# Kernel optimization log

Hardware: AMD Instinct MI355X
Metric: run time of the kernel (lower is better)

## Reference

```python
import jax, jax.numpy as jnp
import numpy as np
import math

B, T, D = 2, 2048, 1024
H, HS = 16, 64  # n_heads, head_size; D == H*HS


def setup_inputs() -> dict:
    key = jax.random.key(0)
    k1, k2, k3 = jax.random.split(key, 3)
    x = jax.random.normal(k1, (B, T, D), dtype=jnp.float32)
    w_qkv = jax.random.normal(k2, (D, 3 * D), dtype=jnp.float32) * (1.0 / math.sqrt(D))
    b_qkv = jnp.zeros((3 * D,), dtype=jnp.float32)
    w_out = jax.random.normal(k3, (D, D), dtype=jnp.float32) * (1.0 / math.sqrt(D))
    b_out = jnp.zeros((D,), dtype=jnp.float32)
    return {"x": x, "w_qkv": w_qkv, "b_qkv": b_qkv, "w_out": w_out, "b_out": b_out}


def reference(x, w_qkv, b_qkv, w_out, b_out):
    b, t, d = x.shape
    qkv = x @ w_qkv + b_qkv                       # (B,T,3D)
    q, k, v = jnp.split(qkv, 3, axis=-1)
    # (B,T,D) -> (B,H,T,HS)
    q = q.reshape(b, t, H, HS).transpose(0, 2, 1, 3)
    k = k.reshape(b, t, H, HS).transpose(0, 2, 1, 3)
    v = v.reshape(b, t, H, HS).transpose(0, 2, 1, 3)
    scale = 1.0 / math.sqrt(HS)
    attn = jnp.einsum('bhqd,bhkd->bhqk', q, k) * scale  # (B,H,T,T)
    causal = jnp.tril(jnp.ones((t, t), dtype=bool))
    attn = jnp.where(causal[None, None], attn, -jnp.inf)
    attn = jax.nn.softmax(attn, axis=-1)
    o = jnp.einsum('bhqk,bhkd->bhqd', attn, v)          # (B,H,T,HS)
    o = o.transpose(0, 2, 1, 3).reshape(b, t, d)
    return o @ w_out + b_out
```

## Files before the change

### kernel.cpp

```cpp
#include <hip/hip_runtime.h>
#include <math.h>

#define B_  2
#define T_  2048
#define D_  1024
#define H_  16
#define HS_ 64
#define M_  (B_*T_)

typedef __bf16 bf16x8 __attribute__((ext_vector_type(8)));
typedef float  f32x4  __attribute__((ext_vector_type(4)));
typedef unsigned short u16;

static __device__ __forceinline__ u16 f2bf(float f) {
    unsigned int u = __float_as_uint(f);
    u += 0x7fff + ((u >> 16) & 1);
    return (u16)(u >> 16);
}

static __device__ __forceinline__ void glds16(const u16* g, u16* l) {
    __builtin_amdgcn_global_load_lds(
        (const __attribute__((address_space(1))) void*)g,
        (__attribute__((address_space(3))) void*)l, 16, 0, 0);
}

static __device__ __forceinline__ bf16x8 lds_chunk(const u16* base, int row, int c) {
    return *reinterpret_cast<const bf16x8*>(base + (size_t)(row * 8 + (c ^ (row & 7))) * 8);
}

__global__ void cast_kernel(const float* __restrict__ in, u16* __restrict__ out) {
    int i = (blockIdx.x * blockDim.x + threadIdx.x) * 4;
    float4 v = *reinterpret_cast<const float4*>(in + i);
    ushort4 o;
    o.x = f2bf(v.x); o.y = f2bf(v.y); o.z = f2bf(v.z); o.w = f2bf(v.w);
    *reinterpret_cast<ushort4*>(out + i) = o;
}

__global__ void transpose_cast(const float* __restrict__ in, u16* __restrict__ out,
                               int R, int C) {
    __shared__ float tile[32][33];
    int c0 = blockIdx.x * 32, r0 = blockIdx.y * 32;
    int tx = threadIdx.x, ty = threadIdx.y;
    #pragma unroll
    for (int j = 0; j < 4; ++j)
        tile[ty + j*8][tx] = in[(size_t)(r0 + ty + j*8) * C + c0 + tx];
    __syncthreads();
    #pragma unroll
    for (int j = 0; j < 4; ++j)
        out[(size_t)(c0 + ty + j*8) * R + r0 + tx] = f2bf(tile[tx][ty + j*8]);
}

template<int MODE>
__global__ __launch_bounds__(256) void gemm_bt(
    const u16* __restrict__ A, const u16* __restrict__ Bt,
    const float* __restrict__ bias,
    float* __restrict__ Cf,
    u16* __restrict__ Qb, u16* __restrict__ Kb, u16* __restrict__ Vt,
    int M, int N, int K)
{
    __shared__ u16 As[128 * 64];
    __shared__ u16 Bs[128 * 64];
    int tid  = threadIdx.x;
    int lane = tid & 63, wave = tid >> 6;
    int wm = wave >> 1, wn = wave & 1;
    int quad = lane >> 4, lr = lane & 15;
    int bm = blockIdx.x, bn = blockIdx.y;

    f32x4 acc[4][4] = {};

    const u16* Ab = A  + (size_t)(bm * 128) * K;
    const u16* Bb = Bt + (size_t)(bn * 128) * K;

    int srow = tid >> 3;
    int scol = ((tid & 7) ^ (srow & 7)) * 8;

    for (int k0 = 0; k0 < K; k0 += 64) {
        __syncthreads();
        #pragma unroll
        for (int t = 0; t < 4; ++t)
            glds16(Ab + (size_t)(srow + 32*t) * K + k0 + scol, As + (size_t)(tid + 256*t) * 8);
        #pragma unroll
        for (int t = 0; t < 4; ++t)
            glds16(Bb + (size_t)(srow + 32*t) * K + k0 + scol, Bs + (size_t)(tid + 256*t) * 8);
        __syncthreads();
        #pragma unroll
        for (int kk = 0; kk < 2; ++kk) {
            bf16x8 af[4], bfr[4];
            int c = kk * 4 + quad;
            #pragma unroll
            for (int i = 0; i < 4; ++i)
                af[i] = lds_chunk(As, wm*64 + i*16 + lr, c);
            #pragma unroll
            for (int j = 0; j < 4; ++j)
                bfr[j] = lds_chunk(Bs, wn*64 + j*16 + lr, c);
            #pragma unroll
            for (int i = 0; i < 4; ++i)
                #pragma unroll
                for (int j = 0; j < 4; ++j)
                    acc[i][j] = __builtin_amdgcn_mfma_f32_16x16x32_bf16(af[i], bfr[j], acc[i][j], 0, 0, 0);
        }
    }

    #pragma unroll
    for (int i = 0; i < 4; ++i) {
        int mrow = bm*128 + wm*64 + i*16 + quad*4;
        #pragma unroll
        for (int j = 0; j < 4; ++j) {
            int ncol = bn*128 + wn*64 + j*16 + lr;
            float bv = bias[ncol];
            #pragma unroll
            for (int r = 0; r < 4; ++r) {
                float v = acc[i][j][r] + bv;
                int m = mrow + r;
                if (MODE == 1) {
                    Cf[(size_t)m * N + ncol] = v;
                } else {
                    int b = m >> 11, t = m & (T_ - 1);
                    int s = ncol >> 10, rem = ncol & 1023;
                    int h = rem >> 6, d = rem & 63;
                    int bh = b * H_ + h;
                    if (s == 0)      Qb[((size_t)bh*T_ + t)*HS_ + d] = f2bf(v * 0.125f);
                    else if (s == 1) Kb[((size_t)bh*T_ + t)*HS_ + d] = f2bf(v);
                    else             Vt[((size_t)bh*HS_ + d)*T_ + t] = f2bf(v);
                }
            }
        }
    }
}

__global__ __launch_bounds__(256) void attn_kernel(
    const u16* __restrict__ Qb, const u16* __restrict__ Kb,
    const u16* __restrict__ Vt, u16* __restrict__ Ob)
{
    __shared__ u16 Ks[64 * 64];
    __shared__ u16 Vs[64 * 64];
    __shared__ u16 Ps[4][32 * 64];

    int tid  = threadIdx.x;
    int lane = tid & 63, wave = tid >> 6;
    int quad = lane >> 4, lr = lane & 15;

    int lin = blockIdx.x;
    int bh  = (lin & 7) + 8 * ((lin >> 3) & 3);
    int p   = lin >> 5;

    int grp  = wave >> 1;
    int wg   = wave & 1;
    int myst = grp ? (31 - p) : p;
    int qb   = myst * 64 + wg * 32;
    int jd   = myst;
    int jmax = 31 - p;

    bf16x8 qf[2][2];
    #pragma unroll
    for (int mi = 0; mi < 2; ++mi)
        #pragma unroll
        for (int h2 = 0; h2 < 2; ++h2)
            qf[mi][h2] = *reinterpret_cast<const bf16x8*>(
                Qb + ((size_t)bh*T_ + qb + mi*16 + lr)*HS_ + h2*32 + quad*8);

    f32x4 Oa[2][4] = {};
    float lrow[2][4] = {};

    int srow = tid >> 3;
    int scol = ((tid & 7) ^ (srow & 7)) * 8;
    const u16* Kst0 = Kb + ((size_t)bh*T_ + srow     )*HS_ + scol;
    const u16* Kst1 = Kb + ((size_t)bh*T_ + srow + 32)*HS_ + scol;
    const u16* Vst0 = Vt + ((size_t)bh*HS_ + srow     )*T_ + scol;
    const u16* Vst1 = Vt + ((size_t)bh*HS_ + srow + 32)*T_ + scol;

    bf16x8 kpre0 = *reinterpret_cast<const bf16x8*>(Kst0);
    bf16x8 kpre1 = *reinterpret_cast<const bf16x8*>(Kst1);
    bf16x8 vpre0 = *reinterpret_cast<const bf16x8*>(Vst0);
    bf16x8 vpre1 = *reinterpret_cast<const bf16x8*>(Vst1);

    for (int jt = 0; jt <= jmax; ++jt) {
        __syncthreads();
        reinterpret_cast<bf16x8*>(Ks)[tid]       = kpre0;
        reinterpret_cast<bf16x8*>(Ks)[tid + 256] = kpre1;
        reinterpret_cast<bf16x8*>(Vs)[tid]       = vpre0;
        reinterpret_cast<bf16x8*>(Vs)[tid + 256] = vpre1;
        if (jt < jmax) {
            size_t kn = (size_t)(jt + 1) * 64;
            kpre0 = *reinterpret_cast<const bf16x8*>(Kst0 + kn * HS_);
            kpre1 = *reinterpret_cast<const bf16x8*>(Kst1 + kn * HS_);
            vpre0 = *reinterpret_cast<const bf16x8*>(Vst0 + kn);
            vpre1 = *reinterpret_cast<const bf16x8*>(Vst1 + kn);
        }
        __syncthreads();

        if (jt <= jd) {
            int kb = jt * 64;
            f32x4 Sa[2][4] = {};
            #pragma unroll
            for (int kk = 0; kk < 2; ++kk) {
                int c = kk * 4 + quad;
                #pragma unroll
                for (int nt = 0; nt < 4; ++nt) {
                    bf16x8 bk = lds_chunk(Ks, nt*16 + lr, c);
                    #pragma unroll
                    for (int mi = 0; mi < 2; ++mi)
                        Sa[mi][nt] = __builtin_amdgcn_mfma_f32_16x16x32_bf16(
                            qf[mi][kk], bk, Sa[mi][nt], 0, 0, 0);
                }
            }

            if (jt == jd) {
                #pragma unroll
                for (int mi = 0; mi < 2; ++mi)
                    #pragma unroll
                    for (int nt = 0; nt < 4; ++nt)
                        #pragma unroll
                        for (int r = 0; r < 4; ++r) {
                            int kg = kb + nt*16 + lr;
                            int qg = qb + mi*16 + quad*4 + r;
                            if (kg > qg) Sa[mi][nt][r] = -INFINITY;
                        }
            }

            #pragma unroll
            for (int mi = 0; mi < 2; ++mi)
                #pragma unroll
                for (int nt = 0; nt < 4; ++nt)
                    #pragma unroll
                    for (int r = 0; r < 4; ++r) {
                        float pv = __expf(Sa[mi][nt][r]);
                        lrow[mi][r] += pv;
                        int prow = mi*16 + quad*4 + r;
                        int c = nt*2 + (lr >> 3);
                        Ps[wave][(size_t)(prow*8 + (c ^ (prow & 7)))*8 + (lr & 7)] = f2bf(pv);
                    }

            #pragma unroll
            for (int kk = 0; kk < 2; ++kk) {
                int c = kk * 4 + quad;
                bf16x8 pa[2];
                #pragma unroll
                for (int mi = 0; mi < 2; ++mi)
                    pa[mi] = lds_chunk(Ps[wave], mi*16 + lr, c);
                #pragma unroll
                for (int nt = 0; nt < 4; ++nt) {
                    bf16x8 vb = lds_chunk(Vs, nt*16 + lr, c);
                    #pragma unroll
                    for (int mi = 0; mi < 2; ++mi)
                        Oa[mi][nt] = __builtin_amdgcn_mfma_f32_16x16x32_bf16(
                            pa[mi], vb, Oa[mi][nt], 0, 0, 0);
                }
            }
        }
    }

    int b = bh >> 4, h = bh & 15;
    #pragma unroll
    for (int mi = 0; mi < 2; ++mi)
        #pragma unroll
        for (int r = 0; r < 4; ++r) {
            float s = lrow[mi][r];
            #pragma unroll
            for (int off = 8; off >= 1; off >>= 1)
                s += __shfl_xor(s, off, 64);
            float inv = 1.f / s;
            int qg = qb + mi*16 + quad*4 + r;
            #pragma unroll
            for (int nt = 0; nt < 4; ++nt) {
                int d = nt*16 + lr;
                Ob[((size_t)b*T_ + qg)*D_ + h*HS_ + d] = f2bf(Oa[mi][nt][r] * inv);
            }
        }
}

extern "C" void kernel_launch(void* const* d_in, const int* in_sizes, int n_in,
                              void* d_out, int out_size, void* d_ws, size_t ws_size,
                              hipStream_t stream) {
    (void)in_sizes; (void)n_in; (void)out_size; (void)ws_size;
    const float* x     = (const float*)d_in[0];
    const float* w_qkv = (const float*)d_in[1];
    const float* b_qkv = (const float*)d_in[2];
    const float* w_out = (const float*)d_in[3];
    const float* b_out = (const float*)d_in[4];
    float* out = (float*)d_out;

    char* ws = (char*)d_ws;
    u16* Xb    = (u16*)ws; ws += (size_t)M_ * D_ * 2;
    u16* WqkvT = (u16*)ws; ws += (size_t)3 * D_ * D_ * 2;
    u16* WoutT = (u16*)ws; ws += (size_t)D_ * D_ * 2;
    u16* Qb    = (u16*)ws; ws += (size_t)M_ * D_ * 2;
    u16* Kb    = (u16*)ws; ws += (size_t)M_ * D_ * 2;
    u16* Vt    = (u16*)ws; ws += (size_t)M_ * D_ * 2;
    u16* Ob    = (u16*)ws; ws += (size_t)M_ * D_ * 2;

    cast_kernel<<<M_ * D_ / 1024, 256, 0, stream>>>(x, Xb);
    transpose_cast<<<dim3(3*D_/32, D_/32), dim3(32, 8), 0, stream>>>(w_qkv, WqkvT, D_, 3*D_);
    transpose_cast<<<dim3(D_/32,   D_/32), dim3(32, 8), 0, stream>>>(w_out, WoutT, D_, D_);
    gemm_bt<0><<<dim3(M_/128, 3*D_/128), 256, 0, stream>>>(
        Xb, WqkvT, b_qkv, nullptr, Qb, Kb, Vt, M_, 3*D_, D_);
    attn_kernel<<<512, 256, 0, stream>>>(Qb, Kb, Vt, Ob);
    gemm_bt<1><<<dim3(M_/128, D_/128), 256, 0, stream>>>(
        Ob, WoutT, b_out, out, nullptr, nullptr, nullptr, M_, D_, D_);
}
```

Baseline: 210.0 us.

## Merge prep casts into one kernel and halve GEMM K-tile to 32

Replaces the three separate cast/transpose-cast launches with a single prep kernel. It dispatches on block index and uses float4 loads and ushort4 stores for the transposes. Separately, the GEMM K-step drops from 64 to 32 with a new 4-chunk LDS swizzle. This halves shared memory per block, which may raise occupancy, but doubles the number of loop iterations and barriers.

```diff
diff --git a/kernel.cpp b/kernel.cpp
--- a/kernel.cpp
+++ b/kernel.cpp
@@ -24,30 +24,48 @@
         (__attribute__((address_space(3))) void*)l, 16, 0, 0);
 }
 
+static __device__ __forceinline__ bf16x8 lds_chunk4(const u16* base, int row, int c) {
+    return *reinterpret_cast<const bf16x8*>(base + (size_t)(row * 4 + (c ^ ((row >> 1) & 3))) * 8);
+}
+
 static __device__ __forceinline__ bf16x8 lds_chunk(const u16* base, int row, int c) {
     return *reinterpret_cast<const bf16x8*>(base + (size_t)(row * 8 + (c ^ (row & 7))) * 8);
 }
 
-__global__ void cast_kernel(const float* __restrict__ in, u16* __restrict__ out) {
-    int i = (blockIdx.x * blockDim.x + threadIdx.x) * 4;
-    float4 v = *reinterpret_cast<const float4*>(in + i);
+__global__ __launch_bounds__(256) void prep_kernel(
+    const float* __restrict__ x, const float* __restrict__ w_qkv,
+    const float* __restrict__ w_out,
+    u16* __restrict__ Xb, u16* __restrict__ WqkvT, u16* __restrict__ WoutT)
+{
+    int bid = blockIdx.x;
+    if (bid < 4096) {
+        int i = (bid * 256 + threadIdx.x) * 4;
+        float4 v = *reinterpret_cast<const float4*>(x + i);
+        ushort4 o;
+        o.x = f2bf(v.x); o.y = f2bf(v.y); o.z = f2bf(v.z); o.w = f2bf(v.w);
+        *reinterpret_cast<ushort4*>(Xb + i) = o;
+        return;
+    }
+    const float* in; u16* out; int C; int c0, r0;
+    if (bid < 4096 + 3072) {
+        int t = bid - 4096;
+        in = w_qkv; out = WqkvT; C = 3 * D_;
+        c0 = (t % 96) * 32; r0 = (t / 96) * 32;
+    } else {
+        int t = bid - 7168;
+        in = w_out; out = WoutT; C = D_;
+        c0 = (t & 31) * 32; r0 = (t >> 5) * 32;
+    }
+    __shared__ float tile[32][33];
+    int tr = threadIdx.x >> 3, tc4 = (threadIdx.x & 7) * 4;
+    float4 v = *reinterpret_cast<const float4*>(in + (size_t)(r0 + tr) * C + c0 + tc4);
+    tile[tr][tc4+0] = v.x; tile[tr][tc4+1] = v.y;
+    tile[tr][tc4+2] = v.z; tile[tr][tc4+3] = v.w;
+    __syncthreads();
     ushort4 o;
-    o.x = f2bf(v.x); o.y = f2bf(v.y); o.z = f2bf(v.z); o.w = f2bf(v.w);
-    *reinterpret_cast<ushort4*>(out + i) = o;
-}
-
-__global__ void transpose_cast(const float* __restrict__ in, u16* __restrict__ out,
-                               int R, int C) {
-    __shared__ float tile[32][33];
-    int c0 = blockIdx.x * 32, r0 = blockIdx.y * 32;
-    int tx = threadIdx.x, ty = threadIdx.y;
-    #pragma unroll
-    for (int j = 0; j < 4; ++j)
-        tile[ty + j*8][tx] = in[(size_t)(r0 + ty + j*8) * C + c0 + tx];
-    __syncthreads();
-    #pragma unroll
-    for (int j = 0; j < 4; ++j)
-        out[(size_t)(c0 + ty + j*8) * R + r0 + tx] = f2bf(tile[tx][ty + j*8]);
+    o.x = f2bf(tile[tc4+0][tr]); o.y = f2bf(tile[tc4+1][tr]);
+    o.z = f2bf(tile[tc4+2][tr]); o.w = f2bf(tile[tc4+3][tr]);
+    *reinterpret_cast<ushort4*>(out + (size_t)(c0 + tr) * D_ + r0 + tc4) = o;
 }
 
 template<int MODE>
@@ -58,8 +76,8 @@
     u16* __restrict__ Qb, u16* __restrict__ Kb, u16* __restrict__ Vt,
     int M, int N, int K)
 {
-    __shared__ u16 As[128 * 64];
-    __shared__ u16 Bs[128 * 64];
+    __shared__ u16 As[128 * 32];
+    __shared__ u16 Bs[128 * 32];
     int tid  = threadIdx.x;
     int lane = tid & 63, wave = tid >> 6;
     int wm = wave >> 1, wn = wave & 1;
@@ -71,34 +89,28 @@
     const u16* Ab = A  + (size_t)(bm * 128) * K;
     const u16* Bb = Bt + (size_t)(bn * 128) * K;
 
-    int srow = tid >> 3;
-    int scol = ((tid & 7) ^ (srow & 7)) * 8;
-
-    for (int k0 = 0; k0 < K; k0 += 64) {
+    int r0 = tid >> 2,         c0 = (((tid) & 3) ^ ((tid >> 3) & 3)) * 8;
+    int r1 = (tid + 256) >> 2, c1 = (((tid + 256) & 3) ^ (((tid + 256) >> 3) & 3)) * 8;
+
+    for (int k0 = 0; k0 < K; k0 += 32) {
         __syncthreads();
-        #pragma unroll
-        for (int t = 0; t < 4; ++t)
-            glds16(Ab + (size_t)(srow + 32*t) * K + k0 + scol, As + (size_t)(tid + 256*t) * 8);
-        #pragma unroll
-        for (int t = 0; t < 4; ++t)
-            glds16(Bb + (size_t)(srow + 32*t) * K + k0 + scol, Bs + (size_t)(tid + 256*t) * 8);
+        glds16(Ab + (size_t)r0 * K + k0 + c0, As + (size_t)tid * 8);
+        glds16(Ab + (size_t)r1 * K + k0 + c1, As + (size_t)(tid + 256) * 8);
+        glds16(Bb + (size_t)r0 * K + k0 + c0, Bs + (size_t)tid * 8);
+        glds16(Bb + (size_t)r1 * K + k0 + c1, Bs + (size_t)(tid + 256) * 8);
         __syncthreads();
-        #pragma unroll
-        for (int kk = 0; kk < 2; ++kk) {
-            bf16x8 af[4], bfr[4];
-            int c = kk * 4 + quad;
-            #pragma unroll
-            for (int i = 0; i < 4; ++i)
-                af[i] = lds_chunk(As, wm*64 + i*16 + lr, c);
+        bf16x8 af[4], bfr[4];
+        #pragma unroll
+        for (int i = 0; i < 4; ++i)
+            af[i] = lds_chunk4(As, wm*64 + i*16 + lr, quad);
+        #pragma unroll
+        for (int j = 0; j < 4; ++j)
+            bfr[j] = lds_chunk4(Bs, wn*64 + j*16 + lr, quad);
+        #pragma unroll
+        for (int i = 0; i < 4; ++i)
             #pragma unroll
             for (int j = 0; j < 4; ++j)
-                bfr[j] = lds_chunk(Bs, wn*64 + j*16 + lr, c);
-            #pragma unroll
-            for (int i = 0; i < 4; ++i)
-                #pragma unroll
-                for (int j = 0; j < 4; ++j)
-                    acc[i][j] = __builtin_amdgcn_mfma_f32_16x16x32_bf16(af[i], bfr[j], acc[i][j], 0, 0, 0);
-        }
+                acc[i][j] = __builtin_amdgcn_mfma_f32_16x16x32_bf16(af[i], bfr[j], acc[i][j], 0, 0, 0);
     }
 
     #pragma unroll
@@ -289,9 +301,7 @@
     u16* Vt    = (u16*)ws; ws += (size_t)M_ * D_ * 2;
     u16* Ob    = (u16*)ws; ws += (size_t)M_ * D_ * 2;
 
-    cast_kernel<<<M_ * D_ / 1024, 256, 0, stream>>>(x, Xb);
-    transpose_cast<<<dim3(3*D_/32, D_/32), dim3(32, 8), 0, stream>>>(w_qkv, WqkvT, D_, 3*D_);
-    transpose_cast<<<dim3(D_/32,   D_/32), dim3(32, 8), 0, stream>>>(w_out, WoutT, D_, D_);
+    prep_kernel<<<8192, 256, 0, stream>>>(x, w_qkv, w_out, Xb, WqkvT, WoutT);
     gemm_bt<0><<<dim3(M_/128, 3*D_/128), 256, 0, stream>>>(
         Xb, WqkvT, b_qkv, nullptr, Qb, Kb, Vt, M_, 3*D_, D_);
     attn_kernel<<<512, 256, 0, stream>>>(Qb, Kb, Vt, Ob);
```

Measured after the change: 206.4 us. About the same (-1.7%).
